# Performance work log

Measured on AMD Instinct MI355X. Metric: run time of the kernel, lower is better.

The kernel has to match this reference:

```python
import jax, jax.numpy as jnp
import numpy as np

N_NODES = 50000
N_EDGES = 800000
IN_CH = 128
HID = 128
OUT_CH = 1
N_GRAPHS = 512


def setup_inputs() -> dict:
    key = jax.random.key(0)
    ks = jax.random.split(key, 8)
    x = jax.random.normal(ks[0], (N_NODES, IN_CH), dtype=jnp.float32)
    edge_index = jax.random.randint(ks[1], (2, N_EDGES), 0, N_NODES, dtype=jnp.int64)
    batch = jnp.sort(jax.random.randint(ks[2], (N_NODES,), 0, N_GRAPHS, dtype=jnp.int64))
    s1 = 1.0 / np.sqrt(IN_CH)
    s2 = 1.0 / np.sqrt(HID)
    W1 = jax.random.normal(ks[3], (IN_CH, HID), dtype=jnp.float32) * s1
    b1 = jnp.zeros((HID,), dtype=jnp.float32)
    W2 = jax.random.normal(ks[4], (HID, HID), dtype=jnp.float32) * s2
    b2 = jnp.zeros((HID,), dtype=jnp.float32)
    Wfc = jax.random.normal(ks[5], (HID, OUT_CH), dtype=jnp.float32) * s2
    bfc = jnp.zeros((OUT_CH,), dtype=jnp.float32)
    return {"x": x, "edge_index": edge_index, "batch": batch,
            "W1": W1, "b1": b1, "W2": W2, "b2": b2, "Wfc": Wfc, "bfc": bfc}


def _gcn_conv(x, W, b, src, dst):
    # PyG GCNConv: add self-loops, symmetric deg^{-1/2} normalization,
    # linear transform, scatter-add aggregation, then bias.
    n = x.shape[0]
    xw = x @ W  # [N, H]
    loop = jnp.arange(n, dtype=src.dtype)
    src2 = jnp.concatenate([src, loop])
    dst2 = jnp.concatenate([dst, loop])
    deg = jax.ops.segment_sum(jnp.ones_like(dst2, dtype=xw.dtype), dst2, num_segments=n)
    dinv = jnp.where(deg > 0, jax.lax.rsqrt(deg), 0.0)
    norm = dinv[src2] * dinv[dst2]  # [E+N]
    msg = xw[src2] * norm[:, None]  # gather + scale, dominant memory traffic
    out = jax.ops.segment_sum(msg, dst2, num_segments=n)
    return out + b


def reference(x, edge_index, batch, W1, b1, W2, b2, Wfc, bfc):
    src, dst = edge_index[0], edge_index[1]
    h = jax.nn.relu(_gcn_conv(x, W1, b1, src, dst))
    h = jax.nn.relu(_gcn_conv(h, W2, b2, src, dst))
    # global mean pool over graphs
    sums = jax.ops.segment_sum(h, batch, num_segments=N_GRAPHS)
    cnts = jax.ops.segment_sum(jnp.ones((h.shape[0],), dtype=h.dtype), batch, num_segments=N_GRAPHS)
    pooled = sums / jnp.maximum(cnts, 1.0)[:, None]
    return pooled @ Wfc + bfc
```

## Files before the change

### kernel.cpp

```cpp
#include <hip/hip_runtime.h>
#include <hip/hip_bf16.h>

typedef float f2 __attribute__((ext_vector_type(2)));
typedef float f4 __attribute__((ext_vector_type(4)));
typedef _Float16 hf;
typedef hf hf2 __attribute__((ext_vector_type(2)));
typedef hf hf4 __attribute__((ext_vector_type(4)));

#define N_NODES 50000
#define N_EDGES 800000
#define CH 128
#define N_GRAPHS 512

__global__ __launch_bounds__(256) void deg_hist_k(const int* __restrict__ dst,
                                                  int* __restrict__ deg) {
    int e = blockIdx.x * 256 + threadIdx.x;
    if (e < N_EDGES) atomicAdd(&deg[dst[e]], 1);
}

__global__ __launch_bounds__(1024) void scan1_k(const int* __restrict__ deg,
                                                int* __restrict__ tmp,
                                                int* __restrict__ bsum, int n) {
    __shared__ int s[1024];
    int tid = threadIdx.x;
    int gid = blockIdx.x * 1024 + tid;
    int v = (gid < n) ? deg[gid] : 0;
    s[tid] = v;
    __syncthreads();
    for (int off = 1; off < 1024; off <<= 1) {
        int t = (tid >= off) ? s[tid - off] : 0;
        __syncthreads();
        s[tid] += t;
        __syncthreads();
    }
    if (gid < n) tmp[gid] = s[tid];
    if (tid == 1023) bsum[blockIdx.x] = s[tid];
}

__global__ void scan2_k(int* __restrict__ bsum, int nb) {
    int lane = threadIdx.x;
    int v = (lane < nb) ? bsum[lane] : 0;
    for (int off = 1; off < 64; off <<= 1) {
        int t = __shfl_up(v, off);
        if (lane >= off) v += t;
    }
    if (lane < nb) bsum[lane] = v;
}

__global__ __launch_bounds__(1024) void scan3_k(const int* __restrict__ tmp,
                                                const int* __restrict__ bsum,
                                                const int* __restrict__ deg,
                                                int* __restrict__ rowp,
                                                int* __restrict__ cursor,
                                                float* __restrict__ dinv, int n) {
    int gid = blockIdx.x * 1024 + threadIdx.x;
    if (gid >= n) return;
    int off = blockIdx.x ? bsum[blockIdx.x - 1] : 0;
    int incl = tmp[gid] + off;
    rowp[gid + 1] = incl;
    cursor[gid] = incl - deg[gid];
    dinv[gid] = rsqrtf((float)deg[gid] + 1.0f);
    if (gid == 0) rowp[0] = 0;
}

__global__ __launch_bounds__(256) void csr_fill_k(const int* __restrict__ src,
                                                  const int* __restrict__ dst,
                                                  int* __restrict__ cursor,
                                                  int* __restrict__ csr) {
    int e = blockIdx.x * 256 + threadIdx.x;
    if (e < N_EDGES) {
        int d = dst[e];
        int pos = atomicAdd(&cursor[d], 1);
        csr[pos] = src[e];
    }
}

template <typename TA>
__global__ __launch_bounds__(256) void gemm_scaled_k(const TA* __restrict__ A,
                                                     const float* __restrict__ W,
                                                     const float* __restrict__ dinv,
                                                     hf* __restrict__ out, int M) {
    __shared__ float sA[64][132];
    __shared__ float sW[128][68];
    int tid = threadIdx.x;
    int row0 = blockIdx.x * 64;
    int col0 = blockIdx.y * 64;

    #pragma unroll
    for (int rep = 0; rep < 8; ++rep) {
        int idx = rep * 256 + tid;
        int r = idx >> 5, k4 = idx & 31;
        f4 vf = {0.f, 0.f, 0.f, 0.f};
        int row = row0 + r;
        if (row < M) {
            if constexpr (sizeof(TA) == 4) {
                vf = *(const f4*)&A[row * 128 + k4 * 4];
            } else {
                hf4 v = *(const hf4*)&A[row * 128 + k4 * 4];
                vf = f4{(float)v[0], (float)v[1], (float)v[2], (float)v[3]};
            }
        }
        *(f4*)&sA[r][k4 * 4] = vf;
    }
    #pragma unroll
    for (int rep = 0; rep < 8; ++rep) {
        int idx = rep * 256 + tid;
        int k = idx >> 4, c4 = idx & 15;
        f4 v = *(const f4*)&W[k * 128 + col0 + c4 * 4];
        *(f4*)&sW[k][c4 * 4] = v;
    }
    __syncthreads();

    int tx = tid & 15, ty = tid >> 4;
    float acc[4][4] = {};
    for (int k = 0; k < 128; k += 4) {
        f4 a[4], b[4];
        #pragma unroll
        for (int i = 0; i < 4; ++i) a[i] = *(const f4*)&sA[ty * 4 + i][k];
        #pragma unroll
        for (int kk = 0; kk < 4; ++kk) b[kk] = *(const f4*)&sW[k + kk][tx * 4];
        #pragma unroll
        for (int i = 0; i < 4; ++i)
            #pragma unroll
            for (int j = 0; j < 4; ++j)
                acc[i][j] += a[i][0] * b[0][j] + a[i][1] * b[1][j] +
                             a[i][2] * b[2][j] + a[i][3] * b[3][j];
    }
    #pragma unroll
    for (int i = 0; i < 4; ++i) {
        int row = row0 + ty * 4 + i;
        if (row < M) {
            float dv = dinv[row];
            hf4 o = {(hf)(acc[i][0] * dv), (hf)(acc[i][1] * dv),
                     (hf)(acc[i][2] * dv), (hf)(acc[i][3] * dv)};
            *(hf4*)&out[row * 128 + col0 + tx * 4] = o;
        }
    }
}

#define ACC4(v) do { acc[0] += (float)(v)[0]; acc[1] += (float)(v)[1]; \
                     acc[2] += (float)(v)[2]; acc[3] += (float)(v)[3]; } while (0)

__device__ __forceinline__ f4 gather_half(const hf4* __restrict__ rows,
                                          const int* __restrict__ rowp,
                                          const int* __restrict__ csr,
                                          int node, int lane) {
    int hl = lane & 31;
    int hbase = lane & 32;
    int beg = rowp[node], end = rowp[node + 1];
    int cnt = end - beg + 1;
    int myE = node;
    if (hl > 0) {
        int j = beg + hl - 1;
        if (j < end) myE = csr[j];
    }
    f4 acc = {0.f, 0.f, 0.f, 0.f};
    int pre = cnt < 32 ? cnt : 32;
    int e = 0;
    for (; e + 8 <= pre; e += 8) {
        int s0 = __shfl(myE, hbase + e + 0);
        int s1 = __shfl(myE, hbase + e + 1);
        int s2 = __shfl(myE, hbase + e + 2);
        int s3 = __shfl(myE, hbase + e + 3);
        int s4 = __shfl(myE, hbase + e + 4);
        int s5 = __shfl(myE, hbase + e + 5);
        int s6 = __shfl(myE, hbase + e + 6);
        int s7 = __shfl(myE, hbase + e + 7);
        hf4 v0 = rows[s0 * 32 + hl];
        hf4 v1 = rows[s1 * 32 + hl];
        hf4 v2 = rows[s2 * 32 + hl];
        hf4 v3 = rows[s3 * 32 + hl];
        hf4 v4 = rows[s4 * 32 + hl];
        hf4 v5 = rows[s5 * 32 + hl];
        hf4 v6 = rows[s6 * 32 + hl];
        hf4 v7 = rows[s7 * 32 + hl];
        ACC4(v0); ACC4(v1); ACC4(v2); ACC4(v3);
        ACC4(v4); ACC4(v5); ACC4(v6); ACC4(v7);
    }
    if (e + 4 <= pre) {
        int s0 = __shfl(myE, hbase + e + 0);
        int s1 = __shfl(myE, hbase + e + 1);
        int s2 = __shfl(myE, hbase + e + 2);
        int s3 = __shfl(myE, hbase + e + 3);
        hf4 v0 = rows[s0 * 32 + hl];
        hf4 v1 = rows[s1 * 32 + hl];
        hf4 v2 = rows[s2 * 32 + hl];
        hf4 v3 = rows[s3 * 32 + hl];
        ACC4(v0); ACC4(v1); ACC4(v2); ACC4(v3);
        e += 4;
    }
    for (; e < pre; ++e) {
        int s0 = __shfl(myE, hbase + e);
        hf4 v0 = rows[s0 * 32 + hl];
        ACC4(v0);
    }
    for (int j = beg + 31; j < end; ++j) {
        int s = csr[j];
        hf4 v = rows[s * 32 + hl];
        ACC4(v);
    }
    return acc;
}

__global__ __launch_bounds__(256) void gather1_k(const hf* __restrict__ xws,
                                                 const float* __restrict__ dinv,
                                                 const int* __restrict__ rowp,
                                                 const int* __restrict__ csr,
                                                 const float* __restrict__ bias,
                                                 hf* __restrict__ h) {
    int node = blockIdx.x * 8 + (threadIdx.x >> 5);
    if (node >= N_NODES) return;
    int lane = threadIdx.x & 63;
    int hl = lane & 31;
    f4 acc = gather_half((const hf4*)xws, rowp, csr, node, lane);
    float dn = dinv[node];
    f4 bb = *(const f4*)&bias[hl * 4];
    hf4 o;
    #pragma unroll
    for (int k = 0; k < 4; ++k)
        o[k] = (hf)fmaxf(acc[k] * dn + bb[k], 0.f);
    ((hf4*)h)[node * 32 + hl] = o;
}

__global__ __launch_bounds__(256) void gather2_pool_k(const hf* __restrict__ xws,
                                                      const float* __restrict__ dinv,
                                                      const int* __restrict__ rowp,
                                                      const int* __restrict__ csr,
                                                      const float* __restrict__ bias,
                                                      const int* __restrict__ batch,
                                                      const float* __restrict__ Wfc,
                                                      float* __restrict__ pool,
                                                      float* __restrict__ cnt) {
    int node = blockIdx.x * 8 + (threadIdx.x >> 5);
    if (node >= N_NODES) return;
    int lane = threadIdx.x & 63;
    int hl = lane & 31;
    f4 acc = gather_half((const hf4*)xws, rowp, csr, node, lane);
    float dn = dinv[node];
    f4 bb = *(const f4*)&bias[hl * 4];
    f4 wf = *(const f4*)&Wfc[hl * 4];
    float p = 0.f;
    #pragma unroll
    for (int k = 0; k < 4; ++k)
        p += fmaxf(acc[k] * dn + bb[k], 0.f) * wf[k];
    #pragma unroll
    for (int off = 16; off > 0; off >>= 1) p += __shfl_xor(p, off);
    if (hl == 0) {
        int g = batch[node];
        atomicAdd(&pool[g], p);
        atomicAdd(&cnt[g], 1.0f);
    }
}

__global__ void finalize_k(const float* __restrict__ pool,
                           const float* __restrict__ cnt,
                           const float* __restrict__ bfc,
                           float* __restrict__ out) {
    int g = blockIdx.x * blockDim.x + threadIdx.x;
    if (g < N_GRAPHS) out[g] = pool[g] / fmaxf(cnt[g], 1.0f) + bfc[0];
}

extern "C" void kernel_launch(void* const* d_in, const int* in_sizes, int n_in,
                              void* d_out, int out_size, void* d_ws, size_t ws_size,
                              hipStream_t stream) {
    const float* x    = (const float*)d_in[0];
    const int*   ei   = (const int*)d_in[1];
    const int*   batch= (const int*)d_in[2];
    const float* W1   = (const float*)d_in[3];
    const float* b1   = (const float*)d_in[4];
    const float* W2   = (const float*)d_in[5];
    const float* b2   = (const float*)d_in[6];
    const float* Wfc  = (const float*)d_in[7];
    const float* bfc  = (const float*)d_in[8];
    float* out = (float*)d_out;

    const int* src = ei;
    const int* dst = ei + N_EDGES;

    char* w = (char*)d_ws;
    float* dinv   = (float*)w; w += 50048 * 4;
    int*   deg    = (int*)w;   w += 50048 * 4;
    int*   rowp   = (int*)w;   w += 50176 * 4;
    int*   cursor = (int*)w;   w += 50048 * 4;
    int*   stmp   = (int*)w;   w += 50048 * 4;
    int*   bsum   = (int*)w;   w += 256 * 4;
    int*   csr    = (int*)w;   w += N_EDGES * 4;
    hf*    xws1   = (hf*)w;    w += (size_t)N_NODES * 128 * 2;
    hf*    h1     = (hf*)w;    w += (size_t)N_NODES * 128 * 2;
    hf*    xws2   = (hf*)w;    w += (size_t)N_NODES * 128 * 2;
    float* pool   = (float*)w; w += 512 * 4;
    float* cnt    = (float*)w; w += 512 * 4;

    hipMemsetAsync(deg, 0, N_NODES * sizeof(int), stream);
    hipMemsetAsync(pool, 0, 2 * 512 * sizeof(float), stream);

    int eb = (N_EDGES + 255) / 256;
    deg_hist_k<<<eb, 256, 0, stream>>>(dst, deg);

    int nb = (N_NODES + 1023) / 1024;
    scan1_k<<<nb, 1024, 0, stream>>>(deg, stmp, bsum, N_NODES);
    scan2_k<<<1, 64, 0, stream>>>(bsum, nb);
    scan3_k<<<nb, 1024, 0, stream>>>(stmp, bsum, deg, rowp, cursor, dinv, N_NODES);

    csr_fill_k<<<eb, 256, 0, stream>>>(src, dst, cursor, csr);

    dim3 ggrid((N_NODES + 63) / 64, 2);
    gemm_scaled_k<float><<<ggrid, 256, 0, stream>>>(x, W1, dinv, xws1, N_NODES);

    int gb = (N_NODES + 7) / 8;
    gather1_k<<<gb, 256, 0, stream>>>(xws1, dinv, rowp, csr, b1, h1);

    gemm_scaled_k<hf><<<ggrid, 256, 0, stream>>>(h1, W2, dinv, xws2, N_NODES);

    gather2_pool_k<<<gb, 256, 0, stream>>>(xws2, dinv, rowp, csr, b2, batch, Wfc,
                                           pool, cnt);

    finalize_k<<<2, 256, 0, stream>>>(pool, cnt, bfc, out);
}
```

Measured before the change: 363.3 us.

## Replace FP32 shared-memory GEMM with MFMA f16 GEMM using prepacked weight fragments

Replaces the scalar FP32 tiled GEMM with a wavefront-level MFMA 16x16x32 f16 kernel. Weights are pre-packed into per-lane fragments by a small kernel, and A rows are loaded directly from global memory without shared memory. The input x is converted to f16 on the fly, which lowers precision. The gather launches also drop the bounds check, relying on N_NODES being divisible by 8. Output stores become scattered 2-byte writes, which may cost bandwidth.

```diff
diff --git a/kernel.cpp b/kernel.cpp
--- a/kernel.cpp
+++ b/kernel.cpp
@@ -6,6 +6,7 @@
 typedef _Float16 hf;
 typedef hf hf2 __attribute__((ext_vector_type(2)));
 typedef hf hf4 __attribute__((ext_vector_type(4)));
+typedef hf hf8 __attribute__((ext_vector_type(8)));
 
 #define N_NODES 50000
 #define N_EDGES 800000
@@ -75,65 +76,72 @@
     }
 }
 
-template <typename TA>
-__global__ __launch_bounds__(256) void gemm_scaled_k(const TA* __restrict__ A,
-                                                     const float* __restrict__ W,
-                                                     const float* __restrict__ dinv,
-                                                     hf* __restrict__ out, int M) {
-    __shared__ float sA[64][132];
-    __shared__ float sW[128][68];
-    int tid = threadIdx.x;
-    int row0 = blockIdx.x * 64;
-    int col0 = blockIdx.y * 64;
-
-    #pragma unroll
-    for (int rep = 0; rep < 8; ++rep) {
-        int idx = rep * 256 + tid;
-        int r = idx >> 5, k4 = idx & 31;
-        f4 vf = {0.f, 0.f, 0.f, 0.f};
-        int row = row0 + r;
-        if (row < M) {
-            if constexpr (sizeof(TA) == 4) {
-                vf = *(const f4*)&A[row * 128 + k4 * 4];
+__global__ __launch_bounds__(256) void wfrag_k(const float* __restrict__ W,
+                                               hf* __restrict__ frag) {
+    int gid = blockIdx.x * 256 + threadIdx.x;
+    if (gid >= 2048) return;
+    int lane = gid & 63, kc = (gid >> 6) & 3, ct = gid >> 8;
+    int c = ct * 16 + (lane & 15);
+    int k0 = kc * 32 + ((lane >> 4) & 3) * 8;
+    hf8 v;
+    #pragma unroll
+    for (int j = 0; j < 8; ++j) v[j] = (hf)W[(k0 + j) * 128 + c];
+    ((hf8*)frag)[gid] = v;
+}
+
+template <bool CVT>
+__global__ __launch_bounds__(256) void gemm_mfma_k(const void* __restrict__ Av,
+                                                   const hf* __restrict__ wfrag,
+                                                   const float* __restrict__ dinv,
+                                                   hf* __restrict__ out, int M) {
+    int wid = threadIdx.x >> 6, lane = threadIdx.x & 63;
+    int r0 = blockIdx.x * 128 + wid * 32;
+    int rA = lane & 15, g = (lane >> 4) & 3;
+    f4 acc[2][8] = {};
+
+    for (int kc = 0; kc < 4; ++kc) {
+        int k0 = kc * 32 + g * 8;
+        hf8 a0, a1;
+        {
+            int row = r0 + rA;      if (row > M - 1) row = M - 1;
+            int row2 = r0 + 16 + rA; if (row2 > M - 1) row2 = M - 1;
+            if constexpr (CVT) {
+                const float* ap = (const float*)Av;
+                f4 lo = *(const f4*)&ap[(size_t)row * 128 + k0];
+                f4 hi = *(const f4*)&ap[(size_t)row * 128 + k0 + 4];
+                a0 = hf8{(hf)lo[0], (hf)lo[1], (hf)lo[2], (hf)lo[3],
+                         (hf)hi[0], (hf)hi[1], (hf)hi[2], (hf)hi[3]};
+                f4 lo2 = *(const f4*)&ap[(size_t)row2 * 128 + k0];
+                f4 hi2 = *(const f4*)&ap[(size_t)row2 * 128 + k0 + 4];
+                a1 = hf8{(hf)lo2[0], (hf)lo2[1], (hf)lo2[2], (hf)lo2[3],
+                         (hf)hi2[0], (hf)hi2[1], (hf)hi2[2], (hf)hi2[3]};
             } else {
-                hf4 v = *(const hf4*)&A[row * 128 + k4 * 4];
-                vf = f4{(float)v[0], (float)v[1], (float)v[2], (float)v[3]};
+                const hf* ap = (const hf*)Av;
+                a0 = *(const hf8*)&ap[(size_t)row * 128 + k0];
+                a1 = *(const hf8*)&ap[(size_t)row2 * 128 + k0];
             }
         }
-        *(f4*)&sA[r][k4 * 4] = vf;
-    }
-    #pragma unroll
-    for (int rep = 0; rep < 8; ++rep) {
-        int idx = rep * 256 + tid;
-        int k = idx >> 4, c4 = idx & 15;
-        f4 v = *(const f4*)&W[k * 128 + col0 + c4 * 4];
-        *(f4*)&sW[k][c4 * 4] = v;
-    }
-    __syncthreads();
-
-    int tx = tid & 15, ty = tid >> 4;
-    float acc[4][4] = {};
-    for (int k = 0; k < 128; k += 4) {
-        f4 a[4], b[4];
         #pragma unroll
-        for (int i = 0; i < 4; ++i) a[i] = *(const f4*)&sA[ty * 4 + i][k];
+        for (int ct = 0; ct < 8; ++ct) {
+            hf8 b = *(const hf8*)&wfrag[(size_t)((ct * 4 + kc) * 64 + lane) * 8];
+            acc[0][ct] = __builtin_amdgcn_mfma_f32_16x16x32_f16(a0, b,
+                                                                acc[0][ct], 0, 0, 0);
+            acc[1][ct] = __builtin_amdgcn_mfma_f32_16x16x32_f16(a1, b,
+                                                                acc[1][ct], 0, 0, 0);
+        }
+    }
+    #pragma unroll
+    for (int rt = 0; rt < 2; ++rt) {
         #pragma unroll
-        for (int kk = 0; kk < 4; ++kk) b[kk] = *(const f4*)&sW[k + kk][tx * 4];
-        #pragma unroll
-        for (int i = 0; i < 4; ++i)
-            #pragma unroll
-            for (int j = 0; j < 4; ++j)
-                acc[i][j] += a[i][0] * b[0][j] + a[i][1] * b[1][j] +
-                             a[i][2] * b[2][j] + a[i][3] * b[3][j];
-    }
-    #pragma unroll
-    for (int i = 0; i < 4; ++i) {
-        int row = row0 + ty * 4 + i;
-        if (row < M) {
-            float dv = dinv[row];
-            hf4 o = {(hf)(acc[i][0] * dv), (hf)(acc[i][1] * dv),
-                     (hf)(acc[i][2] * dv), (hf)(acc[i][3] * dv)};
-            *(hf4*)&out[row * 128 + col0 + tx * 4] = o;
+        for (int reg = 0; reg < 4; ++reg) {
+            int row = r0 + rt * 16 + g * 4 + reg;
+            if (row < M) {
+                float dv = dinv[row];
+                #pragma unroll
+                for (int ct = 0; ct < 8; ++ct)
+                    out[(size_t)row * 128 + ct * 16 + rA] =
+                        (hf)(acc[rt][ct][reg] * dv);
+            }
         }
     }
 }
@@ -209,7 +217,6 @@
                                                  const float* __restrict__ bias,
                                                  hf* __restrict__ h) {
     int node = blockIdx.x * 8 + (threadIdx.x >> 5);
-    if (node >= N_NODES) return;
     int lane = threadIdx.x & 63;
     int hl = lane & 31;
     f4 acc = gather_half((const hf4*)xws, rowp, csr, node, lane);
@@ -232,7 +239,6 @@
                                                       float* __restrict__ pool,
                                                       float* __restrict__ cnt) {
     int node = blockIdx.x * 8 + (threadIdx.x >> 5);
-    if (node >= N_NODES) return;
     int lane = threadIdx.x & 63;
     int hl = lane & 31;
     f4 acc = gather_half((const hf4*)xws, rowp, csr, node, lane);
@@ -284,6 +290,8 @@
     int*   cursor = (int*)w;   w += 50048 * 4;
     int*   stmp   = (int*)w;   w += 50048 * 4;
     int*   bsum   = (int*)w;   w += 256 * 4;
+    hf*    wf1    = (hf*)w;    w += 16384 * 2;
+    hf*    wf2    = (hf*)w;    w += 16384 * 2;
     int*   csr    = (int*)w;   w += N_EDGES * 4;
     hf*    xws1   = (hf*)w;    w += (size_t)N_NODES * 128 * 2;
     hf*    h1     = (hf*)w;    w += (size_t)N_NODES * 128 * 2;
@@ -304,13 +312,16 @@
 
     csr_fill_k<<<eb, 256, 0, stream>>>(src, dst, cursor, csr);
 
-    dim3 ggrid((N_NODES + 63) / 64, 2);
-    gemm_scaled_k<float><<<ggrid, 256, 0, stream>>>(x, W1, dinv, xws1, N_NODES);
-
-    int gb = (N_NODES + 7) / 8;
+    wfrag_k<<<8, 256, 0, stream>>>(W1, wf1);
+    wfrag_k<<<8, 256, 0, stream>>>(W2, wf2);
+
+    int mg = (N_NODES + 127) / 128;
+    gemm_mfma_k<true><<<mg, 256, 0, stream>>>(x, wf1, dinv, xws1, N_NODES);
+
+    int gb = N_NODES / 8;
     gather1_k<<<gb, 256, 0, stream>>>(xws1, dinv, rowp, csr, b1, h1);
 
-    gemm_scaled_k<hf><<<ggrid, 256, 0, stream>>>(h1, W2, dinv, xws2, N_NODES);
+    gemm_mfma_k<false><<<mg, 256, 0, stream>>>(h1, wf2, dinv, xws2, N_NODES);
 
     gather2_pool_k<<<gb, 256, 0, stream>>>(xws2, dinv, rowp, csr, b2, batch, Wfc,
                                            pool, cnt);
```

Result: faster. 330.9 us (-8.9%).
